# Kernel optimization log

Hardware: AMD Instinct MI355X
Metric: run time of the kernel (lower is better)

Reference implementation:

```python
import jax, jax.numpy as jnp
import numpy as np
from jax import lax

B, T, C, H, N = 4, 1024, 2048, 32, 64
KVH = 8            # kv heads -> kv_dim = 512, n_rep = 4
GN_EPS = 0.00064   # group_norm eps from Step3


def _l2norm(x):
    # torch F.normalize(p=2, dim=-1) with eps=1e-12
    n = jnp.linalg.norm(x, axis=-1, keepdims=True)
    return x / jnp.maximum(n, 1e-12)


def _rwkv7_scan(r, decay, k, v, aa, bb, state):
    # all inputs (B,T,H,N); state (B,H,N,N) with layout [value, key]
    def step(S, inp):
        r_t, d_t, k_t, v_t, a_t, b_t = inp  # each (B,H,N)
        sa = jnp.einsum('bhik,bhk->bhi', S, a_t)
        S = (S * d_t[:, :, None, :]
             + sa[..., None] * b_t[:, :, None, :]
             + v_t[..., None] * k_t[:, :, None, :])
        y = jnp.einsum('bhik,bhk->bhi', S, r_t)
        return S, y
    xs = tuple(jnp.moveaxis(t, 1, 0) for t in (r, decay, k, v, aa, bb))  # (T,B,H,N)
    state, ys = lax.scan(step, state, xs)
    return jnp.moveaxis(ys, 0, 1), state  # (B,T,H,N), (B,H,N,N)


def _forward(x, v_first, state, R, R_bias, K, K_bias, V, V_bias, O, O_bias,
             w0, w1, w2, a0, a1, a2, v0, v1, v2, k_k, k_a, r_k, ln_w, ln_b):
    # ---- Step1: projections + gates (hybrid_matmul -> plain matmul in fp32 ref) ----
    r = x @ R.T + R_bias                                   # (B,T,C)
    w_raw = -jax.nn.softplus(-(w0 + jnp.tanh(x @ w1) @ w2)) - 0.6
    k = x @ K.T + K_bias                                   # (B,T,512)
    v = x @ V.T + V_bias
    n_rep = C // K.shape[0]
    k = jnp.repeat(k.reshape(B, T, KVH, N), n_rep, axis=2).reshape(B, T, C)
    v = jnp.repeat(v.reshape(B, T, KVH, N), n_rep, axis=2).reshape(B, T, C)
    a = jax.nn.sigmoid(a0 + (x @ a1) @ a2)
    kk = _l2norm((k * k_k).reshape(B, T, H, N)).reshape(B, T, C)
    k = k * (1.0 + (a - 1.0) * k_a)
    # layer_id != 0: cross-layer value blending
    v = v + (v_first - v) * jax.nn.sigmoid(v0 + (x @ v1) @ v2)
    aa = -kk
    bb = kk * a
    # ---- Step2: fused recurrent rwkv7 (fp32 state) ----
    decay = jnp.exp(-jnp.exp(w_raw.astype(jnp.float32)))
    rs = lambda t: t.astype(jnp.float32).reshape(B, T, H, N)
    y, state_out = _rwkv7_scan(rs(r), decay.reshape(B, T, H, N), rs(k), rs(v), rs(aa), rs(bb), state)
    # ---- Step3: group norm over (T, N) per (batch, head) as in the (B,C,T) permute ----
    mean = y.mean(axis=(1, 3), keepdims=True)
    var = ((y - mean) ** 2).mean(axis=(1, 3), keepdims=True)
    yn = (y - mean) * lax.rsqrt(var + GN_EPS)
    xx = (yn * ln_w.reshape(H, N) + ln_b.reshape(H, N)).reshape(B, T, C)
    bonus = ((r.reshape(B, T, H, N) * k.reshape(B, T, H, N) * r_k.reshape(H, N))
             .sum(-1, keepdims=True) * v.reshape(B, T, H, N)).reshape(B, T, C)
    xx = xx + bonus
    out = xx @ O.T + O_bias
    return out


def setup_inputs() -> dict:
    key = jax.random.key(0)
    ks = jax.random.split(key, 25)
    g = lambda i, shape, s: jax.random.normal(ks[i], shape, dtype=jnp.float32) * s
    return {
        'x': g(0, (B, T, C), 1.0),
        'v_first': g(1, (B, T, C), 1.0),
        'state': jnp.zeros((B, H, N, N), dtype=jnp.float32),
        'R': g(2, (C, C), 0.02), 'R_bias': jnp.zeros((C,), jnp.float32),
        'K': g(3, (KVH * N, C), 0.02), 'K_bias': jnp.zeros((KVH * N,), jnp.float32),
        'V': g(4, (KVH * N, C), 0.02), 'V_bias': jnp.zeros((KVH * N,), jnp.float32),
        'O': g(5, (C, C), 0.02), 'O_bias': jnp.zeros((C,), jnp.float32),
        'w0': g(6, (C,), 0.1), 'w1': g(7, (C, 64), 0.05), 'w2': g(8, (64, C), 0.05),
        'a0': g(9, (C,), 0.1), 'a1': g(10, (C, 64), 0.05), 'a2': g(11, (64, C), 0.05),
        'v0': g(12, (C,), 0.1), 'v1': g(13, (C, 32), 0.05), 'v2': g(14, (32, C), 0.05),
        'k_k': 1.0 + g(15, (C,), 0.05),
        'k_a': 1.0 + g(16, (C,), 0.05),
        'r_k': g(17, (C,), 0.1),
        'ln_w': jnp.ones((C,), jnp.float32),
        'ln_b': jnp.zeros((C,), jnp.float32),
    }


def reference(x, v_first, state, R, R_bias, K, K_bias, V, V_bias, O, O_bias,
              w0, w1, w2, a0, a1, a2, v0, v1, v2, k_k, k_a, r_k, ln_w, ln_b):
    return _forward(x, v_first, state, R, R_bias, K, K_bias, V, V_bias, O, O_bias,
                    w0, w1, w2, a0, a1, a2, v0, v1, v2, k_k, k_a, r_k, ln_w, ln_b)
```

## Files before the change

kernel.cpp:

```cpp
#include <hip/hip_runtime.h>
#include <hip/hip_bf16.h>
#include <math.h>

typedef __attribute__((ext_vector_type(8))) short bf16x8;
typedef __attribute__((ext_vector_type(4))) float f32x4;

__device__ __forceinline__ unsigned short f2b(float f) {
  unsigned u = __float_as_uint(f);
  unsigned r = (u + 0x7FFF + ((u >> 16) & 1)) >> 16;
  return (unsigned short)r;
}

__device__ __forceinline__ void async16(const void* g, void* l) {
  __builtin_amdgcn_global_load_lds(
      (const __attribute__((address_space(1))) unsigned int*)(g),
      (__attribute__((address_space(3))) unsigned int*)(l), 16, 0, 0);
}

__device__ __forceinline__ float rowsum16(float x) {
  x += __int_as_float(__builtin_amdgcn_update_dpp(0, __float_as_int(x), 0x121, 0xF, 0xF, false));
  x += __int_as_float(__builtin_amdgcn_update_dpp(0, __float_as_int(x), 0x122, 0xF, 0xF, false));
  x += __int_as_float(__builtin_amdgcn_update_dpp(0, __float_as_int(x), 0x124, 0xF, 0xF, false));
  x += __int_as_float(__builtin_amdgcn_update_dpp(0, __float_as_int(x), 0x128, 0xF, 0xF, false));
  return x;
}

__device__ __forceinline__ float mixhi(float a, unsigned pk, float c) {
  float d;
  asm("v_fma_mix_f32 %0, %1, %2, %3 op_sel:[0,1,0] op_sel_hi:[0,1,0]"
      : "=v"(d) : "v"(a), "v"(pk), "v"(c));
  return d;
}
__device__ __forceinline__ float mixlo(float a, unsigned pk, float c) {
  float d;
  asm("v_fma_mix_f32 %0, %1, %2, %3 op_sel:[0,0,0] op_sel_hi:[0,1,0]"
      : "=v"(d) : "v"(a), "v"(pk), "v"(c));
  return d;
}
__device__ __forceinline__ float h2f(unsigned h) {
  float f; asm("v_cvt_f32_f16 %0, %1" : "=v"(f) : "v"(h)); return f;
}

__global__ __launch_bounds__(256) void cvt4_kernel(
    const float* __restrict__ x, const float* __restrict__ R,
    const float* __restrict__ K, const float* __restrict__ V,
    unsigned short* __restrict__ xb, unsigned short* __restrict__ RKVb)
{
  const int bid = blockIdx.x;
  const float* s; unsigned short* d; int i;
  if (bid < 8192)       { s = x; d = xb; i = bid * 256 + threadIdx.x; }
  else if (bid < 12288) { s = R; d = RKVb; i = (bid - 8192) * 256 + threadIdx.x; }
  else if (bid < 13312) { s = K; d = RKVb + 2048 * 2048; i = (bid - 12288) * 256 + threadIdx.x; }
  else                  { s = V; d = RKVb + 2560 * 2048; i = (bid - 13312) * 256 + threadIdx.x; }
  float4 v = ((const float4*)s)[i];
  ushort4 o;
  o.x = f2b(v.x); o.y = f2b(v.y); o.z = f2b(v.z); o.w = f2b(v.w);
  ((ushort4*)d)[i] = o;
}

__global__ __launch_bounds__(256) void cvt_bf16(
    const float* __restrict__ s, unsigned short* __restrict__ d, int n4)
{
  int i = blockIdx.x * 256 + threadIdx.x;
  if (i < n4) {
    float4 v = ((const float4*)s)[i];
    ushort4 o;
    o.x = f2b(v.x); o.y = f2b(v.y); o.z = f2b(v.z); o.w = f2b(v.w);
    ((ushort4*)d)[i] = o;
  }
}

__global__ __launch_bounds__(256) void tcvt_all(
    const float* __restrict__ w1, const float* __restrict__ a1,
    const float* __restrict__ v1, const float* __restrict__ w2,
    const float* __restrict__ a2, const float* __restrict__ v2,
    unsigned short* __restrict__ Bcat, unsigned short* __restrict__ w2t,
    unsigned short* __restrict__ a2t, unsigned short* __restrict__ v2t)
{
  const int r = blockIdx.x >> 5, i = blockIdx.x & 31;
  const float* in; unsigned short* out; int Kd, Nd, ors, bx, by;
  switch (r) {
    case 0:  in = w1; out = Bcat;             Kd = 2048; Nd = 64;   ors = 2048; bx = 0; by = i; break;
    case 1:  in = a1; out = Bcat + 64 * 2048; Kd = 2048; Nd = 64;   ors = 2048; bx = 0; by = i; break;
    case 2:  in = v1; out = Bcat + 128 * 2048; Kd = 2048; Nd = 32;  ors = 2048; bx = 0; by = i; break;
    case 3:  in = w2; out = w2t;              Kd = 64;   Nd = 2048; ors = 64;   bx = i; by = 0; break;
    case 4:  in = a2; out = a2t;              Kd = 64;   Nd = 2048; ors = 64;   bx = i; by = 0; break;
    default: in = v2; out = v2t;              Kd = 32;   Nd = 2048; ors = 32;   bx = i; by = 0; break;
  }
  __shared__ unsigned short tile[64][65];
  const int tx = threadIdx.x & 63, ty = threadIdx.x >> 6;
  const int n0 = bx * 64, k0 = by * 64;
  #pragma unroll
  for (int j = 0; j < 16; ++j) {
    const int k = k0 + j * 4 + ty;
    const int n = n0 + tx;
    unsigned short v = 0;
    if (k < Kd && n < Nd) v = f2b(in[(size_t)k * Nd + n]);
    tile[j * 4 + ty][tx] = v;
  }
  __syncthreads();
  #pragma unroll
  for (int j = 0; j < 16; ++j) {
    const int n = n0 + j * 4 + ty;
    const int k = k0 + tx;
    if (n < Nd && k < Kd) out[(size_t)n * ors + k] = tile[tx][j * 4 + ty];
  }
}

template<int OUTBF16, int ACT>
__device__ __forceinline__ void gemm_body(
    const unsigned short* __restrict__ A, int lda,
    const unsigned short* __restrict__ B, int ldb,
    const float* __restrict__ bias, void* __restrict__ Cv, int ldc,
    int M, int N, int K, int row0, int col0)
{
  __shared__ __align__(16) unsigned short As[128 * 32];
  __shared__ __align__(16) unsigned short Bs[128 * 32];
  const int tid = threadIdx.x;
  const int w = tid >> 6, lane = tid & 63;
  const int wr = (w >> 1) * 64, wc = (w & 1) * 64;

  f32x4 acc[4][4];
  #pragma unroll
  for (int i = 0; i < 4; ++i)
    #pragma unroll
    for (int j = 0; j < 4; ++j)
      acc[i][j] = (f32x4){0.f, 0.f, 0.f, 0.f};

  const int srow = w * 32 + (lane >> 2);
  const int scol = (lane & 3) * 8;
  const int brow0 = (col0 + srow < N) ? (col0 + srow) : 0;
  const int brow1 = (col0 + srow + 16 < N) ? (col0 + srow + 16) : 0;
  const unsigned short* gA0 = A + (size_t)(row0 + srow) * lda + scol;
  const unsigned short* gA1 = gA0 + (size_t)16 * lda;
  const unsigned short* gB0 = B + (size_t)brow0 * ldb + scol;
  const unsigned short* gB1 = B + (size_t)brow1 * ldb + scol;
  unsigned short* lA0 = As + w * 1024;
  unsigned short* lA1 = As + w * 1024 + 512;
  unsigned short* lB0 = Bs + w * 1024;
  unsigned short* lB1 = Bs + w * 1024 + 512;

  const int m16 = lane & 15;
  const int q8  = (lane >> 4) * 8;

  for (int k0 = 0; k0 < K; k0 += 32) {
    async16(gA0, lA0);
    async16(gA1, lA1);
    async16(gB0, lB0);
    async16(gB1, lB1);
    gA0 += 32; gA1 += 32; gB0 += 32; gB1 += 32;
    __syncthreads();
    bf16x8 af[4], bfr[4];
    #pragma unroll
    for (int i = 0; i < 4; ++i) {
      af[i]  = *(const bf16x8*)(As + (wr + i * 16 + m16) * 32 + q8);
      bfr[i] = *(const bf16x8*)(Bs + (wc + i * 16 + m16) * 32 + q8);
    }
    #pragma unroll
    for (int i = 0; i < 4; ++i)
      #pragma unroll
      for (int j = 0; j < 4; ++j)
        acc[i][j] = __builtin_amdgcn_mfma_f32_16x16x32_bf16(af[i], bfr[j], acc[i][j], 0, 0, 0);
    __syncthreads();
  }

  #pragma unroll
  for (int j = 0; j < 4; ++j) {
    const int c_ = col0 + wc + j * 16 + (lane & 15);
    if (c_ < N) {
      const float bv = bias ? bias[c_] : 0.f;
      #pragma unroll
      for (int i = 0; i < 4; ++i) {
        const int r_ = row0 + wr + i * 16 + (lane >> 4) * 4;
        #pragma unroll
        for (int t4 = 0; t4 < 4; ++t4) {
          float v = acc[i][j][t4] + bv;
          if (ACT == 2 && c_ < 64) v = tanhf(v);
          if (OUTBF16)
            ((unsigned short*)Cv)[(size_t)(r_ + t4) * ldc + c_] = f2b(v);
          else
            ((float*)Cv)[(size_t)(r_ + t4) * ldc + c_] = v;
        }
      }
    }
  }
}

template<int OUTBF16, int ACT>
__global__ __launch_bounds__(256) void gemm_mfma(
    const unsigned short* __restrict__ A, int lda,
    const unsigned short* __restrict__ B, int ldb,
    const float* __restrict__ bias, void* __restrict__ Cv, int ldc,
    int M, int N, int K)
{
  gemm_body<OUTBF16, ACT>(A, lda, B, ldb, bias, Cv, ldc, M, N, K,
                          blockIdx.y * 128, blockIdx.x * 128);
}

__global__ __launch_bounds__(256) void gemm_lr2(
    const unsigned short* __restrict__ hcat,
    const unsigned short* __restrict__ w2t,
    const unsigned short* __restrict__ a2t,
    const unsigned short* __restrict__ v2t,
    float* __restrict__ wt, float* __restrict__ at, float* __restrict__ vt)
{
  const int z = blockIdx.z;
  const unsigned short* A; const unsigned short* Bm; float* C; int K;
  if (z == 0)      { A = hcat;       Bm = w2t; C = wt; K = 64; }
  else if (z == 1) { A = hcat + 64;  Bm = a2t; C = at; K = 64; }
  else             { A = hcat + 128; Bm = v2t; C = vt; K = 32; }
  gemm_body<0, 0>(A, 160, Bm, K, nullptr, C, 2048, 4096, 2048, K,
                  blockIdx.y * 128, blockIdx.x * 128);
}

__global__ __launch_bounds__(256) void gemm_rkv(
    const unsigned short* __restrict__ A, const unsigned short* __restrict__ B,
    const float* __restrict__ Rb_, const float* __restrict__ Kb_,
    const float* __restrict__ Vb_,
    float* __restrict__ Cr, float* __restrict__ Ck, float* __restrict__ Cvv)
{
  const int col0 = blockIdx.x * 128;
  float* Cd; int ldc, cbase; const float* bias;
  if (col0 < 2048)      { Cd = Cr;  ldc = 2048; cbase = col0;        bias = Rb_; }
  else if (col0 < 2560) { Cd = Ck;  ldc = 512;  cbase = col0 - 2048; bias = Kb_; }
  else                  { Cd = Cvv; ldc = 512;  cbase = col0 - 2560; bias = Vb_; }
  __shared__ __align__(16) unsigned short As[128 * 32];
  __shared__ __align__(16) unsigned short Bs[128 * 32];
  const int tid = threadIdx.x;
  const int w = tid >> 6, lane = tid & 63;
  const int wr = (w >> 1) * 64, wc = (w & 1) * 64;
  const int row0 = blockIdx.y * 128;

  f32x4 acc[4][4];
  #pragma unroll
  for (int i = 0; i < 4; ++i)
    #pragma unroll
    for (int j = 0; j < 4; ++j)
      acc[i][j] = (f32x4){0.f, 0.f, 0.f, 0.f};

  const int srow = w * 32 + (lane >> 2);
  const int scol = (lane & 3) * 8;
  const unsigned short* gA0 = A + (size_t)(row0 + srow) * 2048 + scol;
  const unsigned short* gA1 = gA0 + (size_t)16 * 2048;
  const unsigned short* gB0 = B + (size_t)(col0 + srow) * 2048 + scol;
  const unsigned short* gB1 = gB0 + (size_t)16 * 2048;
  unsigned short* lA0 = As + w * 1024;
  unsigned short* lA1 = As + w * 1024 + 512;
  unsigned short* lB0 = Bs + w * 1024;
  unsigned short* lB1 = Bs + w * 1024 + 512;

  const int m16 = lane & 15;
  const int q8  = (lane >> 4) * 8;

  for (int k0 = 0; k0 < 2048; k0 += 32) {
    async16(gA0, lA0);
    async16(gA1, lA1);
    async16(gB0, lB0);
    async16(gB1, lB1);
    gA0 += 32; gA1 += 32; gB0 += 32; gB1 += 32;
    __syncthreads();
    bf16x8 af[4], bfr[4];
    #pragma unroll
    for (int i = 0; i < 4; ++i) {
      af[i]  = *(const bf16x8*)(As + (wr + i * 16 + m16) * 32 + q8);
      bfr[i] = *(const bf16x8*)(Bs + (wc + i * 16 + m16) * 32 + q8);
    }
    #pragma unroll
    for (int i = 0; i < 4; ++i)
      #pragma unroll
      for (int j = 0; j < 4; ++j)
        acc[i][j] = __builtin_amdgcn_mfma_f32_16x16x32_bf16(af[i], bfr[j], acc[i][j], 0, 0, 0);
    __syncthreads();
  }

  #pragma unroll
  for (int j = 0; j < 4; ++j) {
    const int c_ = cbase + wc + j * 16 + (lane & 15);
    const float bv = bias[c_];
    #pragma unroll
    for (int i = 0; i < 4; ++i) {
      const int r_ = row0 + wr + i * 16 + (lane >> 4) * 4;
      #pragma unroll
      for (int t4 = 0; t4 < 4; ++t4)
        Cd[(size_t)(r_ + t4) * ldc + c_] = acc[i][j][t4] + bv;
    }
  }
}

__global__ __launch_bounds__(256) void prep_kernel(
    const float* __restrict__ k_buf, const float* __restrict__ v_buf,
    const float* __restrict__ r_buf,
    float* wt_decay, const float* __restrict__ at, float* vt_vf,
    const float* __restrict__ v_first,
    const float* __restrict__ w0, const float* __restrict__ a0,
    const float* __restrict__ v0, const float* __restrict__ k_k,
    const float* __restrict__ k_a,
    unsigned* __restrict__ rk_pk, unsigned* __restrict__ ab_pk)
{
  const int row = blockIdx.x;
  const int tid = threadIdx.x;
  const int c0 = tid << 3;
  const int h = tid >> 3;
  const int kvoff = (h >> 2) << 6;
  const size_t base = (size_t)row * 2048;
  const size_t kvrow = (size_t)row * 512;
  float kr[8], kkr[8];
  float ss = 0.f;
  #pragma unroll
  for (int e = 0; e < 8; ++e) {
    const int c = c0 + e;
    const float kv = k_buf[kvrow + kvoff + (c & 63)];
    kr[e] = kv;
    const float t = kv * k_k[c];
    kkr[e] = t;
    ss = fmaf(t, t, ss);
  }
  ss += __shfl_xor(ss, 1);
  ss += __shfl_xor(ss, 2);
  ss += __shfl_xor(ss, 4);
  const float inv = 1.f / fmaxf(sqrtf(ss), 1e-12f);
  #pragma unroll
  for (int e = 0; e < 8; ++e) {
    const int c = c0 + e;
    const size_t idx = base + c;
    const float kk = kkr[e] * inv;
    const float a = 1.f / (1.f + expf(-(a0[c] + at[idx])));
    const float u = w0[c] + wt_decay[idx];
    const float sig_u = 1.f / (1.f + expf(-u));
    wt_decay[idx] = expf(-0.5488116360940264f * sig_u);
    const float kfin = kr[e] * fmaf(a - 1.f, k_a[c], 1.f);
    const float vr = v_buf[kvrow + kvoff + (c & 63)];
    const float sv = 1.f / (1.f + expf(-(v0[c] + vt_vf[idx])));
    vt_vf[idx] = vr + (v_first[idx] - vr) * sv;
    const float bbv = kk * a;
    const float aav = -kk;
    unsigned rk_u, ab_u;
    asm("v_cvt_pkrtz_f16_f32 %0, %1, %2" : "=v"(rk_u) : "v"(r_buf[idx]), "v"(kfin));
    asm("v_cvt_pkrtz_f16_f32 %0, %1, %2" : "=v"(ab_u) : "v"(bbv), "v"(aav));
    rk_pk[idx] = rk_u;
    ab_pk[idx] = ab_u;
  }
}

#define WB(n) asm volatile("s_waitcnt vmcnt(" #n ") lgkmcnt(0)\n\ts_barrier" ::: "memory")
#define BAR2() asm volatile("s_waitcnt lgkmcnt(0)\n\ts_barrier" ::: "memory")

__global__ __launch_bounds__(256) void scan_kernel(
    const unsigned* __restrict__ rkB, const unsigned* __restrict__ abB,
    const float* __restrict__ dB, const float* __restrict__ vB,
    const float* __restrict__ state, float* __restrict__ y,
    float* __restrict__ part)
{
  __shared__ float lds[6912];
  unsigned* ldsU = (unsigned*)lds;
  const int tid = threadIdx.x;
  const int bid = blockIdx.x;
  const int xcd = bid & 7, bj = bid >> 3;
  const int m = bj & 3, gq = bj >> 2;
  const int bh = (gq << 3) | xcd;
  const int widx = tid >> 6;
  const int lane = tid & 63;
  const int rg = lane >> 4;
  const int colg = lane & 15;
  const int rowb = (widx << 2) + rg;
  const int row = (m << 4) + rowb;
  const int b = bh >> 5, h = bh & 31;

  float4 S = *(const float4*)(state + (size_t)bh * 4096 + row * 64 + (colg << 2));

  const unsigned cb = (unsigned)((b * 1024) * 2048 + h * 64);
  const unsigned sstep = (unsigned)(tid >> 4);
  const unsigned scol = (unsigned)((tid & 15) << 2);
  const unsigned lseg = (unsigned)(widx << 8);

  float sacc = 0.f, ssacc = 0.f;
  const float fzero = 0.0f;

  #define STAGE(step0, bofs) do {                                            \
    const unsigned go_ = cb + ((step0) + sstep) * 2048u + scol;              \
    async16(rkB + go_, ldsU + (bofs) + lseg);                                \
    async16(abB + go_, ldsU + (bofs) + 1024 + lseg);                         \
    async16(dB + go_,  lds + (bofs) + 2048 + lseg);                          \
    if (lane < 16) {                                                         \
      const unsigned gv_ = cb + ((step0) + (unsigned)(widx << 2)             \
                                 + (unsigned)(lane >> 2)) * 2048u            \
                           + (unsigned)(m << 4) + (unsigned)((lane & 3) << 2); \
      async16(vB + gv_, lds + (bofs) + 3072 + (widx << 6));                  \
    }                                                                        \
  } while (0)

  #define PROCESS(bofs) do {                                                 \
    _Pragma("unroll")                                                        \
    for (int s = 0; s < 16; ++s) {                                           \
      const uint4 rkw = *(const uint4*)(ldsU + (bofs) + s * 64 + (colg << 2)); \
      const uint4 abw = *(const uint4*)(ldsU + (bofs) + 1024 + s * 64 + (colg << 2)); \
      const float4 dv = *(const float4*)(lds + (bofs) + 2048 + s * 64 + (colg << 2)); \
      const float vv = lds[(bofs) + 3072 + (s << 4) + rowb];                 \
      float t0 = mixhi(S.x, abw.x, fzero);                                   \
      t0 = mixhi(S.y, abw.y, t0);                                            \
      t0 = mixhi(S.z, abw.z, t0);                                            \
      t0 = mixhi(S.w, abw.w, t0);                                            \
      const float sa = rowsum16(t0);                                         \
      float p0 = mixhi(vv, rkw.x, fzero);                                    \
      float p1 = mixhi(vv, rkw.y, fzero);                                    \
      float p2 = mixhi(vv, rkw.z, fzero);                                    \
      float p3 = mixhi(vv, rkw.w, fzero);                                    \
      p0 = mixlo(sa, abw.x, p0);                                             \
      p1 = mixlo(sa, abw.y, p1);                                             \
      p2 = mixlo(sa, abw.z, p2);                                             \
      p3 = mixlo(sa, abw.w, p3);                                             \
      S.x = fmaf(S.x, dv.x, p0);                                             \
      S.y = fmaf(S.y, dv.y, p1);                                             \
      S.z = fmaf(S.z, dv.z, p2);                                             \
      S.w = fmaf(S.w, dv.w, p3);                                             \
      float t1 = mixlo(S.x, rkw.x, fzero);                                   \
      t1 = mixlo(S.y, rkw.y, t1);                                            \
      t1 = mixlo(S.z, rkw.z, t1);                                            \
      t1 = mixlo(S.w, rkw.w, t1);                                            \
      const float yv = rowsum16(t1);                                         \
      if (colg == 0) {                                                       \
        lds[6656 + (s << 4) + rowb] = yv;                                    \
        sacc += yv;                                                          \
        ssacc = fmaf(yv, yv, ssacc);                                         \
      }                                                                      \
    }                                                                        \
  } while (0)

  #define YSTORE(step0) do {                                                 \
    const float val_ = lds[6656 + tid];                                      \
    y[cb + ((step0) + (unsigned)(tid >> 4)) * 2048u +                        \
      (unsigned)(m << 4) + (unsigned)(tid & 15)] = val_;                     \
  } while (0)

  STAGE(0u, 0);
  STAGE(16u, 3328);

  WB(4);
  PROCESS(0);
  BAR2();
  YSTORE(0u);
  STAGE(32u, 0);

  for (int c = 1; c <= 62; ++c) {
    const int bofs = (c & 1) ? 3328 : 0;
    WB(5);
    PROCESS(bofs);
    BAR2();
    YSTORE((unsigned)(c << 4));
    if (c < 62) STAGE((unsigned)((c + 2) << 4), bofs);
  }

  WB(1);
  PROCESS(3328);
  BAR2();
  YSTORE(1008u);

  sacc  += __shfl_xor(sacc, 16);
  sacc  += __shfl_xor(sacc, 32);
  ssacc += __shfl_xor(ssacc, 16);
  ssacc += __shfl_xor(ssacc, 32);
  __syncthreads();
  if (lane == 0) { lds[widx] = sacc; lds[4 + widx] = ssacc; }
  __syncthreads();
  if (tid == 0) {
    const float s_  = lds[0] + lds[1] + lds[2] + lds[3];
    const float ss_ = lds[4] + lds[5] + lds[6] + lds[7];
    ((float2*)part)[(bh << 2) + m] = make_float2(s_, ss_);
  }

  #undef STAGE
  #undef PROCESS
  #undef YSTORE
}

__global__ __launch_bounds__(256) void gapply_kernel(
    const float* __restrict__ y, const unsigned* __restrict__ rkB,
    const float* __restrict__ vf,
    const float* __restrict__ part, const float* __restrict__ r_k,
    const float* __restrict__ ln_w, const float* __restrict__ ln_b,
    unsigned short* __restrict__ xxb)
{
  const int row = blockIdx.x;
  const int b = row >> 10;
  const int tid = threadIdx.x;
  const int h = tid >> 3;
  const int bh = b * 32 + h;
  float s = 0.f, ss = 0.f;
  #pragma unroll
  for (int j = 0; j < 4; ++j) {
    const float2 pr = ((const float2*)part)[(bh << 2) + j];
    s += pr.x; ss += pr.y;
  }
  const float mean = s * (1.f / 65536.f);
  const float rstd = rsqrtf(ss * (1.f / 65536.f) - mean * mean + 0.00064f);
  const int c0 = tid << 3;
  const size_t base = (size_t)row * 2048 + c0;
  float yv[8], vv[8];
  float p = 0.f;
  #pragma unroll
  for (int e = 0; e < 8; ++e) {
    yv[e] = y[base + e];
    vv[e] = vf[base + e];
    const unsigned w_ = rkB[base + e];
    p = fmaf(h2f(w_ & 0xffffu) * h2f(w_ >> 16), r_k[c0 + e], p);
  }
  p += __shfl_xor(p, 1);
  p += __shfl_xor(p, 2);
  p += __shfl_xor(p, 4);
  #pragma unroll
  for (int e = 0; e < 8; ++e) {
    const float yn = (yv[e] - mean) * rstd;
    xxb[base + e] = f2b(fmaf(yn, ln_w[c0 + e], ln_b[c0 + e]) + p * vv[e]);
  }
}

extern "C" void kernel_launch(void* const* d_in, const int* in_sizes, int n_in,
                              void* d_out, int out_size, void* d_ws, size_t ws_size,
                              hipStream_t stream) {
  const float* x       = (const float*)d_in[0];
  const float* v_first = (const float*)d_in[1];
  const float* state   = (const float*)d_in[2];
  const float* Rw      = (const float*)d_in[3];
  const float* R_bias  = (const float*)d_in[4];
  const float* Kw      = (const float*)d_in[5];
  const float* K_bias  = (const float*)d_in[6];
  const float* Vw      = (const float*)d_in[7];
  const float* V_bias  = (const float*)d_in[8];
  const float* Ow      = (const float*)d_in[9];
  const float* O_bias  = (const float*)d_in[10];
  const float* w0      = (const float*)d_in[11];
  const float* w1      = (const float*)d_in[12];
  const float* w2      = (const float*)d_in[13];
  const float* a0      = (const float*)d_in[14];
  const float* a1      = (const float*)d_in[15];
  const float* a2      = (const float*)d_in[16];
  const float* v0      = (const float*)d_in[17];
  const float* v1      = (const float*)d_in[18];
  const float* v2      = (const float*)d_in[19];
  const float* k_k     = (const float*)d_in[20];
  const float* k_a     = (const float*)d_in[21];
  const float* r_k     = (const float*)d_in[22];
  const float* ln_w    = (const float*)d_in[23];
  const float* ln_b    = (const float*)d_in[24];

  float* ws = (float*)d_ws;
  float* r_buf = ws;
  float* k_buf = r_buf + 8388608;
  float* v_buf = k_buf + 2097152;
  float* wt    = v_buf + 2097152;
  float* at    = wt    + 8388608;
  float* vt    = at    + 8388608;
  float* kf    = vt    + 8388608;
  float* aaq   = kf    + 8388608;
  float* bbq   = aaq   + 8388608;
  float* part  = bbq   + 8388608;
  unsigned short* xb   = (unsigned short*)bbq;
  unsigned short* RKVb = (unsigned short*)kf;
  unsigned short* hcat = (unsigned short*)(kf + 3200000);
  unsigned short* Bcat = (unsigned short*)(kf + 3600000);
  unsigned short* w2t  = (unsigned short*)(kf + 3800000);
  unsigned short* a2t  = (unsigned short*)(kf + 3900000);
  unsigned short* v2t  = (unsigned short*)(kf + 4000000);
  unsigned* rk_pk      = (unsigned*)aaq;
  unsigned* ab_pk      = (unsigned*)bbq;
  unsigned short* Ob   = (unsigned short*)wt;
  unsigned short* xxb  = (unsigned short*)bbq;

  dim3 blk(256);
  cvt4_kernel<<<14336, blk, 0, stream>>>(x, Rw, Kw, Vw, xb, RKVb);
  tcvt_all<<<192, blk, 0, stream>>>(w1, a1, v1, w2, a2, v2, Bcat, w2t, a2t, v2t);
  gemm_mfma<1,2><<<dim3(2, 32), blk, 0, stream>>>(xb, 2048, Bcat, 2048, nullptr,
                                                  hcat, 160, 4096, 160, 2048);
  gemm_rkv<<<dim3(24, 32), blk, 0, stream>>>(xb, RKVb, R_bias, K_bias, V_bias,
                                             r_buf, k_buf, v_buf);
  gemm_lr2<<<dim3(16, 32, 3), blk, 0, stream>>>(hcat, w2t, a2t, v2t, wt, at, vt);
  prep_kernel<<<4096, blk, 0, stream>>>(k_buf, v_buf, r_buf, wt, at, vt, v_first,
                                        w0, a0, v0, k_k, k_a, rk_pk, ab_pk);
  float* ybuf = at;
  scan_kernel<<<512, blk, 0, stream>>>(rk_pk, ab_pk, wt, vt, state, ybuf, part);
  cvt_bf16<<<4096, blk, 0, stream>>>(Ow, Ob, 1048576);
  gapply_kernel<<<4096, blk, 0, stream>>>(ybuf, rk_pk, vt, part, r_k,
                                          ln_w, ln_b, xxb);
  gemm_mfma<0,0><<<dim3(16, 32), blk, 0, stream>>>(xxb, 2048, Ob, 2048, O_bias,
                                                   (float*)d_out, 2048, 4096, 2048, 2048);
}
```

Measured before the change: 748.4 us.

## Fuse low-rank projection into RKV GEMM, fold O conversion, deepen scan staging

The O weight conversion now runs inside the initial fp32-to-bf16 kernel, and the low-rank x@[w1|a1|v1] GEMM with its tanh epilogue is merged into the R/K/V projection GEMM as extra column blocks. This removes two kernel launches and one separate small GEMM. The scan kernel now stages 32 timesteps per LDS buffer instead of 16 and prefetches the next step's LDS operands into registers while computing the current one. In exchange it doubles LDS use, which may reduce occupancy, and the fused GEMM wastes some work on padded columns past 160.

```diff
diff --git a/kernel.cpp b/kernel.cpp
--- a/kernel.cpp
+++ b/kernel.cpp
@@ -44,30 +44,21 @@
 __global__ __launch_bounds__(256) void cvt4_kernel(
     const float* __restrict__ x, const float* __restrict__ R,
     const float* __restrict__ K, const float* __restrict__ V,
-    unsigned short* __restrict__ xb, unsigned short* __restrict__ RKVb)
+    const float* __restrict__ Ow,
+    unsigned short* __restrict__ xb, unsigned short* __restrict__ RKVb,
+    unsigned short* __restrict__ Ob)
 {
   const int bid = blockIdx.x;
   const float* s; unsigned short* d; int i;
   if (bid < 8192)       { s = x; d = xb; i = bid * 256 + threadIdx.x; }
   else if (bid < 12288) { s = R; d = RKVb; i = (bid - 8192) * 256 + threadIdx.x; }
   else if (bid < 13312) { s = K; d = RKVb + 2048 * 2048; i = (bid - 12288) * 256 + threadIdx.x; }
-  else                  { s = V; d = RKVb + 2560 * 2048; i = (bid - 13312) * 256 + threadIdx.x; }
+  else if (bid < 14336) { s = V; d = RKVb + 2560 * 2048; i = (bid - 13312) * 256 + threadIdx.x; }
+  else                  { s = Ow; d = Ob; i = (bid - 14336) * 256 + threadIdx.x; }
   float4 v = ((const float4*)s)[i];
   ushort4 o;
   o.x = f2b(v.x); o.y = f2b(v.y); o.z = f2b(v.z); o.w = f2b(v.w);
   ((ushort4*)d)[i] = o;
-}
-
-__global__ __launch_bounds__(256) void cvt_bf16(
-    const float* __restrict__ s, unsigned short* __restrict__ d, int n4)
-{
-  int i = blockIdx.x * 256 + threadIdx.x;
-  if (i < n4) {
-    float4 v = ((const float4*)s)[i];
-    ushort4 o;
-    o.x = f2b(v.x); o.y = f2b(v.y); o.z = f2b(v.z); o.w = f2b(v.w);
-    ((ushort4*)d)[i] = o;
-  }
 }
 
 __global__ __launch_bounds__(256) void tcvt_all(
@@ -213,23 +204,27 @@
                   blockIdx.y * 128, blockIdx.x * 128);
 }
 
-__global__ __launch_bounds__(256) void gemm_rkv(
+__global__ __launch_bounds__(256) void gemm_rkvh(
     const unsigned short* __restrict__ A, const unsigned short* __restrict__ B,
     const float* __restrict__ Rb_, const float* __restrict__ Kb_,
     const float* __restrict__ Vb_,
-    float* __restrict__ Cr, float* __restrict__ Ck, float* __restrict__ Cvv)
+    float* __restrict__ Cr, float* __restrict__ Ck, float* __restrict__ Cvv,
+    unsigned short* __restrict__ hcat)
 {
   const int col0 = blockIdx.x * 128;
-  float* Cd; int ldc, cbase; const float* bias;
-  if (col0 < 2048)      { Cd = Cr;  ldc = 2048; cbase = col0;        bias = Rb_; }
-  else if (col0 < 2560) { Cd = Ck;  ldc = 512;  cbase = col0 - 2048; bias = Kb_; }
-  else                  { Cd = Cvv; ldc = 512;  cbase = col0 - 2560; bias = Vb_; }
+  const int row0 = blockIdx.y * 128;
+  float* Cf = nullptr; unsigned short* Ch = nullptr;
+  int ldc, cbase; const float* bias = nullptr;
+  if (col0 < 2048)      { Cf = Cr;  ldc = 2048; cbase = col0;        bias = Rb_; }
+  else if (col0 < 2560) { Cf = Ck;  ldc = 512;  cbase = col0 - 2048; bias = Kb_; }
+  else if (col0 < 3072) { Cf = Cvv; ldc = 512;  cbase = col0 - 2560; bias = Vb_; }
+  else                  { Ch = hcat; ldc = 160; cbase = col0 - 3072; }
+
   __shared__ __align__(16) unsigned short As[128 * 32];
   __shared__ __align__(16) unsigned short Bs[128 * 32];
   const int tid = threadIdx.x;
   const int w = tid >> 6, lane = tid & 63;
   const int wr = (w >> 1) * 64, wc = (w & 1) * 64;
-  const int row0 = blockIdx.y * 128;
 
   f32x4 acc[4][4];
   #pragma unroll
@@ -240,10 +235,12 @@
 
   const int srow = w * 32 + (lane >> 2);
   const int scol = (lane & 3) * 8;
+  const int brow0 = (col0 + srow < 3232) ? (col0 + srow) : 0;
+  const int brow1 = (col0 + srow + 16 < 3232) ? (col0 + srow + 16) : 0;
   const unsigned short* gA0 = A + (size_t)(row0 + srow) * 2048 + scol;
   const unsigned short* gA1 = gA0 + (size_t)16 * 2048;
-  const unsigned short* gB0 = B + (size_t)(col0 + srow) * 2048 + scol;
-  const unsigned short* gB1 = gB0 + (size_t)16 * 2048;
+  const unsigned short* gB0 = B + (size_t)brow0 * 2048 + scol;
+  const unsigned short* gB1 = B + (size_t)brow1 * 2048 + scol;
   unsigned short* lA0 = As + w * 1024;
   unsigned short* lA1 = As + w * 1024 + 512;
   unsigned short* lB0 = Bs + w * 1024;
@@ -276,13 +273,28 @@
   #pragma unroll
   for (int j = 0; j < 4; ++j) {
     const int c_ = cbase + wc + j * 16 + (lane & 15);
-    const float bv = bias[c_];
-    #pragma unroll
-    for (int i = 0; i < 4; ++i) {
-      const int r_ = row0 + wr + i * 16 + (lane >> 4) * 4;
+    if (Ch) {
+      if (c_ < 160) {
+        #pragma unroll
+        for (int i = 0; i < 4; ++i) {
+          const int r_ = row0 + wr + i * 16 + (lane >> 4) * 4;
+          #pragma unroll
+          for (int t4 = 0; t4 < 4; ++t4) {
+            float v = acc[i][j][t4];
+            if (c_ < 64) v = tanhf(v);
+            Ch[(size_t)(r_ + t4) * 160 + c_] = f2b(v);
+          }
+        }
+      }
+    } else {
+      const float bv = bias[c_];
       #pragma unroll
-      for (int t4 = 0; t4 < 4; ++t4)
-        Cd[(size_t)(r_ + t4) * ldc + c_] = acc[i][j][t4] + bv;
+      for (int i = 0; i < 4; ++i) {
+        const int r_ = row0 + wr + i * 16 + (lane >> 4) * 4;
+        #pragma unroll
+        for (int t4 = 0; t4 < 4; ++t4)
+          Cf[(size_t)(r_ + t4) * ldc + c_] = acc[i][j][t4] + bv;
+      }
     }
   }
 }
@@ -351,7 +363,7 @@
     const float* __restrict__ state, float* __restrict__ y,
     float* __restrict__ part)
 {
-  __shared__ float lds[6912];
+  __shared__ float lds[13824];
   unsigned* ldsU = (unsigned*)lds;
   const int tid = threadIdx.x;
   const int bid = blockIdx.x;
@@ -369,57 +381,71 @@
   float4 S = *(const float4*)(state + (size_t)bh * 4096 + row * 64 + (colg << 2));
 
   const unsigned cb = (unsigned)((b * 1024) * 2048 + h * 64);
-  const unsigned sstep = (unsigned)(tid >> 4);
-  const unsigned scol = (unsigned)((tid & 15) << 2);
-  const unsigned lseg = (unsigned)(widx << 8);
+  const unsigned srow8 = (unsigned)((widx << 3) + rg);
+  const unsigned scol = (unsigned)(colg << 2);
+  const unsigned sseg = (unsigned)(widx << 9);
 
   float sacc = 0.f, ssacc = 0.f;
   const float fzero = 0.0f;
 
   #define STAGE(step0, bofs) do {                                            \
-    const unsigned go_ = cb + ((step0) + sstep) * 2048u + scol;              \
-    async16(rkB + go_, ldsU + (bofs) + lseg);                                \
-    async16(abB + go_, ldsU + (bofs) + 1024 + lseg);                         \
-    async16(dB + go_,  lds + (bofs) + 2048 + lseg);                          \
-    if (lane < 16) {                                                         \
-      const unsigned gv_ = cb + ((step0) + (unsigned)(widx << 2)             \
+    const unsigned go0_ = cb + ((step0) + srow8) * 2048u + scol;             \
+    const unsigned go1_ = go0_ + 4u * 2048u;                                 \
+    async16(rkB + go0_, ldsU + (bofs) + sseg);                               \
+    async16(rkB + go1_, ldsU + (bofs) + sseg + 256);                         \
+    async16(abB + go0_, ldsU + (bofs) + 2048 + sseg);                        \
+    async16(abB + go1_, ldsU + (bofs) + 2048 + sseg + 256);                  \
+    async16(dB + go0_,  lds + (bofs) + 4096 + sseg);                         \
+    async16(dB + go1_,  lds + (bofs) + 4096 + sseg + 256);                   \
+    if (lane < 32) {                                                         \
+      const unsigned gv_ = cb + ((step0) + (unsigned)(widx << 3)             \
                                  + (unsigned)(lane >> 2)) * 2048u            \
                            + (unsigned)(m << 4) + (unsigned)((lane & 3) << 2); \
-      async16(vB + gv_, lds + (bofs) + 3072 + (widx << 6));                  \
+      async16(vB + gv_, lds + (bofs) + 6144 + (widx << 7));                  \
     }                                                                        \
   } while (0)
 
   #define PROCESS(bofs) do {                                                 \
+    uint4 rkw = *(const uint4*)(ldsU + (bofs) + (colg << 2));                \
+    uint4 abw = *(const uint4*)(ldsU + (bofs) + 2048 + (colg << 2));         \
+    float4 dvw = *(const float4*)(lds + (bofs) + 4096 + (colg << 2));        \
+    float vvw = lds[(bofs) + 6144 + rowb];                                   \
     _Pragma("unroll")                                                        \
-    for (int s = 0; s < 16; ++s) {                                           \
-      const uint4 rkw = *(const uint4*)(ldsU + (bofs) + s * 64 + (colg << 2)); \
-      const uint4 abw = *(const uint4*)(ldsU + (bofs) + 1024 + s * 64 + (colg << 2)); \
-      const float4 dv = *(const float4*)(lds + (bofs) + 2048 + s * 64 + (colg << 2)); \
-      const float vv = lds[(bofs) + 3072 + (s << 4) + rowb];                 \
-      float t0 = mixhi(S.x, abw.x, fzero);                                   \
-      t0 = mixhi(S.y, abw.y, t0);                                            \
-      t0 = mixhi(S.z, abw.z, t0);                                            \
-      t0 = mixhi(S.w, abw.w, t0);                                            \
+    for (int s = 0; s < 32; ++s) {                                           \
+      const uint4 rkc = rkw;                                                 \
+      const uint4 abc = abw;                                                 \
+      const float4 dvc = dvw;                                                \
+      const float vvc = vvw;                                                 \
+      if (s < 31) {                                                          \
+        rkw = *(const uint4*)(ldsU + (bofs) + (s + 1) * 64 + (colg << 2));   \
+        abw = *(const uint4*)(ldsU + (bofs) + 2048 + (s + 1) * 64 + (colg << 2)); \
+        dvw = *(const float4*)(lds + (bofs) + 4096 + (s + 1) * 64 + (colg << 2)); \
+        vvw = lds[(bofs) + 6144 + ((s + 1) << 4) + rowb];                    \
+      }                                                                      \
+      float t0 = mixhi(S.x, abc.x, fzero);                                   \
+      t0 = mixhi(S.y, abc.y, t0);                                            \
+      t0 = mixhi(S.z, abc.z, t0);                                            \
+      t0 = mixhi(S.w, abc.w, t0);                                            \
       const float sa = rowsum16(t0);                                         \
-      float p0 = mixhi(vv, rkw.x, fzero);                                    \
-      float p1 = mixhi(vv, rkw.y, fzero);                                    \
-      float p2 = mixhi(vv, rkw.z, fzero);                                    \
-      float p3 = mixhi(vv, rkw.w, fzero);                                    \
-      p0 = mixlo(sa, abw.x, p0);                                             \
-      p1 = mixlo(sa, abw.y, p1);                                             \
-      p2 = mixlo(sa, abw.z, p2);                                             \
-      p3 = mixlo(sa, abw.w, p3);                                             \
-      S.x = fmaf(S.x, dv.x, p0);                                             \
-      S.y = fmaf(S.y, dv.y, p1);                                             \
-      S.z = fmaf(S.z, dv.z, p2);                                             \
-      S.w = fmaf(S.w, dv.w, p3);                                             \
-      float t1 = mixlo(S.x, rkw.x, fzero);                                   \
-      t1 = mixlo(S.y, rkw.y, t1);                                            \
-      t1 = mixlo(S.z, rkw.z, t1);                                            \
-      t1 = mixlo(S.w, rkw.w, t1);                                            \
+      float p0 = mixhi(vvc, rkc.x, fzero);                                   \
+      float p1 = mixhi(vvc, rkc.y, fzero);                                   \
+      float p2 = mixhi(vvc, rkc.z, fzero);                                   \
+      float p3 = mixhi(vvc, rkc.w, fzero);                                   \
+      p0 = mixlo(sa, abc.x, p0);                                             \
+      p1 = mixlo(sa, abc.y, p1);                                             \
+      p2 = mixlo(sa, abc.z, p2);                                             \
+      p3 = mixlo(sa, abc.w, p3);                                             \
+      S.x = fmaf(S.x, dvc.x, p0);                                            \
+      S.y = fmaf(S.y, dvc.y, p1);                                            \
+      S.z = fmaf(S.z, dvc.z, p2);                                            \
+      S.w = fmaf(S.w, dvc.w, p3);                                            \
+      float t1 = mixlo(S.x, rkc.x, fzero);                                   \
+      t1 = mixlo(S.y, rkc.y, t1);                                            \
+      t1 = mixlo(S.z, rkc.z, t1);                                            \
+      t1 = mixlo(S.w, rkc.w, t1);                                            \
       const float yv = rowsum16(t1);                                         \
       if (colg == 0) {                                                       \
-        lds[6656 + (s << 4) + rowb] = yv;                                    \
+        lds[13312 + (s << 4) + rowb] = yv;                                   \
         sacc += yv;                                                          \
         ssacc = fmaf(yv, yv, ssacc);                                         \
       }                                                                      \
@@ -427,33 +453,36 @@
   } while (0)
 
   #define YSTORE(step0) do {                                                 \
-    const float val_ = lds[6656 + tid];                                      \
+    const float y0_ = lds[13312 + tid];                                      \
+    const float y1_ = lds[13312 + 256 + tid];                                \
     y[cb + ((step0) + (unsigned)(tid >> 4)) * 2048u +                        \
-      (unsigned)(m << 4) + (unsigned)(tid & 15)] = val_;                     \
+      (unsigned)(m << 4) + (unsigned)(tid & 15)] = y0_;                      \
+    y[cb + ((step0) + 16u + (unsigned)(tid >> 4)) * 2048u +                  \
+      (unsigned)(m << 4) + (unsigned)(tid & 15)] = y1_;                      \
   } while (0)
 
   STAGE(0u, 0);
-  STAGE(16u, 3328);
-
-  WB(4);
+  STAGE(32u, 6656);
+
+  WB(7);
   PROCESS(0);
   BAR2();
   YSTORE(0u);
-  STAGE(32u, 0);
-
-  for (int c = 1; c <= 62; ++c) {
-    const int bofs = (c & 1) ? 3328 : 0;
-    WB(5);
+  STAGE(64u, 0);
+
+  for (int c = 1; c <= 30; ++c) {
+    const int bofs = (c & 1) ? 6656 : 0;
+    WB(9);
     PROCESS(bofs);
     BAR2();
-    YSTORE((unsigned)(c << 4));
-    if (c < 62) STAGE((unsigned)((c + 2) << 4), bofs);
-  }
-
-  WB(1);
-  PROCESS(3328);
+    YSTORE((unsigned)(c << 5));
+    if (c < 30) STAGE((unsigned)((c + 2) << 5), bofs);
+  }
+
+  WB(2);
+  PROCESS(6656);
   BAR2();
-  YSTORE(1008u);
+  YSTORE(992u);
 
   sacc  += __shfl_xor(sacc, 16);
   sacc  += __shfl_xor(sacc, 32);
@@ -556,29 +585,26 @@
   float* part  = bbq   + 8388608;
   unsigned short* xb   = (unsigned short*)bbq;
   unsigned short* RKVb = (unsigned short*)kf;
-  unsigned short* hcat = (unsigned short*)(kf + 3200000);
-  unsigned short* Bcat = (unsigned short*)(kf + 3600000);
+  unsigned short* Bcat = RKVb + 3072 * 2048;
+  unsigned short* hcat = (unsigned short*)(kf + 3400000);
   unsigned short* w2t  = (unsigned short*)(kf + 3800000);
   unsigned short* a2t  = (unsigned short*)(kf + 3900000);
   unsigned short* v2t  = (unsigned short*)(kf + 4000000);
+  unsigned short* Ob   = (unsigned short*)(kf + 4500000);
   unsigned* rk_pk      = (unsigned*)aaq;
   unsigned* ab_pk      = (unsigned*)bbq;
-  unsigned short* Ob   = (unsigned short*)wt;
   unsigned short* xxb  = (unsigned short*)bbq;
 
   dim3 blk(256);
-  cvt4_kernel<<<14336, blk, 0, stream>>>(x, Rw, Kw, Vw, xb, RKVb);
+  cvt4_kernel<<<18432, blk, 0, stream>>>(x, Rw, Kw, Vw, Ow, xb, RKVb, Ob);
   tcvt_all<<<192, blk, 0, stream>>>(w1, a1, v1, w2, a2, v2, Bcat, w2t, a2t, v2t);
-  gemm_mfma<1,2><<<dim3(2, 32), blk, 0, stream>>>(xb, 2048, Bcat, 2048, nullptr,
-                                                  hcat, 160, 4096, 160, 2048);
-  gemm_rkv<<<dim3(24, 32), blk, 0, stream>>>(xb, RKVb, R_bias, K_bias, V_bias,
-                                             r_buf, k_buf, v_buf);
+  gemm_rkvh<<<dim3(26, 32), blk, 0, stream>>>(xb, RKVb, R_bias, K_bias, V_bias,
+                                              r_buf, k_buf, v_buf, hcat);
   gemm_lr2<<<dim3(16, 32, 3), blk, 0, stream>>>(hcat, w2t, a2t, v2t, wt, at, vt);
   prep_kernel<<<4096, blk, 0, stream>>>(k_buf, v_buf, r_buf, wt, at, vt, v_first,
                                         w0, a0, v0, k_k, k_a, rk_pk, ab_pk);
   float* ybuf = at;
   scan_kernel<<<512, blk, 0, stream>>>(rk_pk, ab_pk, wt, vt, state, ybuf, part);
-  cvt_bf16<<<4096, blk, 0, stream>>>(Ow, Ob, 1048576);
   gapply_kernel<<<4096, blk, 0, stream>>>(ybuf, rk_pk, vt, part, r_k,
                                           ln_w, ln_b, xxb);
   gemm_mfma<0,0><<<dim3(16, 32), blk, 0, stream>>>(xxb, 2048, Ob, 2048, O_bias,
```

After: 735.7 us. No clear change (-1.7%).
